# Performance work log

Hardware: AMD Instinct MI355X
Metric: run time of the kernel (lower is better)

Reference implementation:

```python
import jax, jax.numpy as jnp
import numpy as np

D_STATE = 16
DT_RANK = 48
D_CONV = 4
EPS = 1e-5


def rmsnorm(x, w):
    return x * jax.lax.rsqrt(jnp.mean(x * x, axis=-1, keepdims=True) + EPS) * w


def causal_dw_conv(u, w, b):
    # u: [B,T,D], w: [D,K] depthwise causal kernel, b: [D]
    B, T, D = u.shape
    K = w.shape[1]
    up = jnp.pad(u, ((0, 0), (K - 1, 0), (0, 0)))
    acc = jnp.zeros_like(u)
    for k in range(K):  # K=4, tiny fixed loop
        acc = acc + up[:, k:k + T, :] * w[:, k]
    return acc + b


def mamba_mixer(h, ipw, cw, cb, xpw, dpw, dpb, alog, dpar, opw):
    # h: [B,T,d_model]
    B, T, _ = h.shape
    xz = h @ ipw.T                       # [B,T,2*d_inner]
    u, z = jnp.split(xz, 2, axis=-1)     # each [B,T,d_inner]
    u = jax.nn.silu(causal_dw_conv(u, cw, cb))
    xp = u @ xpw.T                       # [B,T,dt_rank+2*d_state]
    dt = xp[..., :DT_RANK]
    Bm = xp[..., DT_RANK:DT_RANK + D_STATE]
    Cm = xp[..., DT_RANK + D_STATE:]
    delta = jax.nn.softplus(dt @ dpw.T + dpb)      # [B,T,d_inner]
    A = -jnp.exp(alog)                              # [d_inner, d_state], negative
    dA = jnp.exp(delta[..., None] * A)              # [B,T,d_inner,d_state] in (0,1)
    dBu = (delta * u)[..., None] * Bm[:, :, None, :]
    # time-major for scan
    dA_t = jnp.moveaxis(dA, 1, 0)
    dBu_t = jnp.moveaxis(dBu, 1, 0)
    C_t = jnp.moveaxis(Cm, 1, 0)

    def step(hst, inp):
        a, bu, c = inp
        hst = a * hst + bu                          # [B,d_inner,d_state]
        y = jnp.einsum('bdn,bn->bd', hst, c)
        return hst, y

    h0 = jnp.zeros((B, u.shape[-1], D_STATE), u.dtype)
    _, ys = jax.lax.scan(step, h0, (dA_t, dBu_t, C_t))
    y = jnp.moveaxis(ys, 0, 1) + u * dpar           # skip via D
    y = y * jax.nn.silu(z)                          # gate
    return y @ opw.T                                # [B,T,d_model]


def setup_inputs() -> dict:
    key = jax.random.key(0)
    ks = jax.random.split(key, 16)
    L, d_model, d_inner = 4, 768, 1536
    B, C, T = 4, 256, 512
    s = 0.02
    return {
        'x': jax.random.normal(ks[0], (B, C, T), jnp.float32),
        'in_proj_w': jax.random.normal(ks[1], (L, 2 * d_inner, d_model), jnp.float32) * s,
        'conv_w': jax.random.normal(ks[2], (L, d_inner, D_CONV), jnp.float32) * 0.3,
        'conv_b': jnp.zeros((L, d_inner), jnp.float32),
        'x_proj_w': jax.random.normal(ks[3], (L, DT_RANK + 2 * D_STATE, d_inner), jnp.float32) * s,
        'dt_proj_w': jax.random.normal(ks[4], (L, d_inner, DT_RANK), jnp.float32) * 0.1,
        'dt_proj_b': jax.random.normal(ks[5], (L, d_inner), jnp.float32) * 0.1 - 4.0,
        'A_log': jax.random.uniform(ks[6], (L, d_inner, D_STATE), jnp.float32, 0.0, 1.5),
        'D_param': jax.random.uniform(ks[7], (L, d_inner), jnp.float32),
        'out_proj_w': jax.random.normal(ks[8], (L, d_model, d_inner), jnp.float32) * s,
        'norm_w': jnp.ones((L, d_model), jnp.float32),
        'norm_f_w': jnp.ones((d_model,), jnp.float32),
        'inp_w': jax.random.normal(ks[9], (d_model, C), jnp.float32) * s,
        'inp_b': jnp.zeros((d_model,), jnp.float32),
        'cls_w': jax.random.normal(ks[10], (10, d_model), jnp.float32) * s,
        'cls_b': jnp.zeros((10,), jnp.float32),
    }


def reference(x, in_proj_w, conv_w, conv_b, x_proj_w, dt_proj_w, dt_proj_b,
              A_log, D_param, out_proj_w, norm_w, norm_f_w,
              inp_w, inp_b, cls_w, cls_b):
    # x: (B, C, T) -> (B, T, C)
    xt = jnp.transpose(x, (0, 2, 1))
    h = xt @ inp_w.T + inp_b                # [B,T,d_model]
    hidden = h
    residual = None
    L = in_proj_w.shape[0]
    for l in range(L):
        residual = hidden if residual is None else hidden + residual
        normed = rmsnorm(residual, norm_w[l])
        hidden = mamba_mixer(normed, in_proj_w[l], conv_w[l], conv_b[l],
                             x_proj_w[l], dt_proj_w[l], dt_proj_b[l],
                             A_log[l], D_param[l], out_proj_w[l])
    residual = hidden + residual
    hidden = rmsnorm(residual, norm_f_w)
    pooled = hidden.mean(axis=1)            # [B,d_model]
    logits = pooled @ cls_w.T + cls_b       # [B,num_labels]
    return logits
```

## Files before the change

kernel.cpp:

```cpp
#include <hip/hip_runtime.h>
#include <math.h>

#define D_MODEL 768
#define D_INNER 1536
#define B_SZ 4
#define T_SZ 512
#define ROWS (B_SZ*T_SZ)
#define XP_N 80
#define CH 16
#define CT 32
#define XS 8
#define XKC (D_INNER/XS)
#define OS 4
#define OKC (D_INNER/OS)
#define MN_OUT (ROWS*768)

typedef __attribute__((ext_vector_type(8))) short bf16x8;
typedef __attribute__((ext_vector_type(4))) float f32x4;

#define GLL(g, l) __builtin_amdgcn_global_load_lds( \
    (const __attribute__((address_space(1))) void*)(g), \
    (__attribute__((address_space(3))) void*)(l), 16, 0, 0)

__device__ __forceinline__ float sigmoidf_(float x){ return 1.0f/(1.0f+__expf(-x)); }
__device__ __forceinline__ float siluf_(float x){ return x*sigmoidf_(x); }
__device__ __forceinline__ unsigned short f2bf(float f){
  unsigned u = __builtin_bit_cast(unsigned, f);
  u = (u + 0x7FFFu + ((u >> 16) & 1u)) >> 16;
  return (unsigned short)u;
}
__device__ __forceinline__ ushort4 cvt4(float4 v){
  ushort4 r; r.x=f2bf(v.x); r.y=f2bf(v.y); r.z=f2bf(v.z); r.w=f2bf(v.w); return r;
}

#define CA_N0 9437184LL
#define CA_N1 4718592LL
#define CA_N2 196608LL
#define CA_N3 786432LL
#define CA_N4 393216LL
__global__ __launch_bounds__(256) void cast_all(
    const float* __restrict__ ipw, unsigned short* __restrict__ wbi,
    const float* __restrict__ opw, unsigned short* __restrict__ wbo,
    const float* __restrict__ inpw, unsigned short* __restrict__ inpwb,
    const float* __restrict__ xpw, unsigned short* __restrict__ xpwb,
    const float* __restrict__ dtw, unsigned short* __restrict__ dtwb)
{
  long long i4 = ((long long)blockIdx.x*256 + threadIdx.x)*4;
  if (i4 < CA_N0){ *(ushort4*)(wbi + i4) = cvt4(*(const float4*)(ipw + i4)); return; }
  i4 -= CA_N0;
  if (i4 < CA_N1){ *(ushort4*)(wbo + i4) = cvt4(*(const float4*)(opw + i4)); return; }
  i4 -= CA_N1;
  if (i4 < CA_N2){ *(ushort4*)(inpwb + i4) = cvt4(*(const float4*)(inpw + i4)); return; }
  i4 -= CA_N2;
  if (i4 < CA_N3){
    const long long l = i4 / (128*1536), rem = i4 % (128*1536);
    const long long r = rem / 1536, k = rem % 1536;
    ushort4 o;
    if (r < 80) o = cvt4(*(const float4*)(xpw + (l*80 + r)*1536 + k));
    else { o.x=0;o.y=0;o.z=0;o.w=0; }
    *(ushort4*)(xpwb + i4) = o; return;
  }
  i4 -= CA_N3;
  if (i4 < CA_N4){
    const long long l = i4 / (1536*64), rem = i4 % (1536*64);
    const long long r = rem / 64, c = rem % 64;
    ushort4 o;
    if (c < 48) o = cvt4(*(const float4*)(dtw + (l*1536 + r)*48 + c));
    else { o.x=0;o.y=0;o.z=0;o.w=0; }
    *(ushort4*)(dtwb + i4) = o;
  }
}

__global__ void transpose_x(const float* __restrict__ x, unsigned short* __restrict__ xtb){
  __shared__ float s[32][33];
  int b = blockIdx.z;
  int t0 = blockIdx.x*32, c0 = blockIdx.y*32;
  int tx = threadIdx.x, ty = threadIdx.y;
  s[ty][tx] = x[((size_t)b*256 + (c0+ty))*512 + (t0+tx)];
  __syncthreads();
  xtb[((size_t)b*512 + (t0+ty))*256 + (c0+tx)] = f2bf(s[tx][ty]);
}

__global__ __launch_bounds__(256) void gemm_bf16(
    const unsigned short* __restrict__ A, const unsigned short* __restrict__ Wb,
    const float* __restrict__ bias,
    float* __restrict__ C, int M, int N, int K)
{
  __shared__ unsigned short As[128*32];
  __shared__ unsigned short Ws[128*32];
  const int tid = threadIdx.x;
  const int bm = blockIdx.y*128, bn = blockIdx.x*128;
  const int wave = tid >> 6, lane = tid & 63;
  const int wm = (wave >> 1)*64, wn = (wave & 1)*64;
  const int fr = lane & 15, quad = lane >> 4;
  f32x4 acc[4][4] = {};
  const int row0 = (wave*64 + lane) >> 2;
  const int khp  = lane & 3;
  const int khl  = (khp + 4 - ((row0 >> 1) & 3)) & 3;
  const unsigned short* Ag = A  + (size_t)(bm + row0)*K + khl*8;
  const unsigned short* Wg = Wb + (size_t)(bn + row0)*K + khl*8;
  const size_t rstep = (size_t)64*K;
  unsigned short* ldsA = As + wave*512;
  unsigned short* ldsW = Ws + wave*512;

  for (int k0 = 0; k0 < K; k0 += 32){
    GLL(Ag + k0,          ldsA);
    GLL(Ag + rstep + k0,  ldsA + 2048);
    GLL(Wg + k0,          ldsW);
    GLL(Wg + rstep + k0,  ldsW + 2048);
    __syncthreads();
    bf16x8 a[4], b[4];
    #pragma unroll
    for (int i=0;i<4;i++){
      const int row = wm + i*16 + fr;
      a[i] = *(const bf16x8*)(As + row*32 + (((quad + (row>>1)) & 3)*8));
    }
    #pragma unroll
    for (int j=0;j<4;j++){
      const int row = wn + j*16 + fr;
      b[j] = *(const bf16x8*)(Ws + row*32 + (((quad + (row>>1)) & 3)*8));
    }
    #pragma unroll
    for (int i=0;i<4;i++)
      #pragma unroll
      for (int j=0;j<4;j++)
        acc[i][j] = __builtin_amdgcn_mfma_f32_16x16x32_bf16(a[i], b[j], acc[i][j], 0, 0, 0);
    __syncthreads();
  }
  #pragma unroll
  for (int i=0;i<4;i++){
    #pragma unroll
    for (int r=0;r<4;r++){
      const int row = bm + wm + i*16 + quad*4 + r;
      float* Cp = C + (size_t)row*N + bn + wn + fr;
      #pragma unroll
      for (int j=0;j<4;j++){
        const int col = bn + wn + j*16 + fr;
        Cp[j*16] = acc[i][j][r] + (bias ? bias[col] : 0.f);
      }
    }
  }
}

__global__ __launch_bounds__(256) void gemm_bf16_sk(
    const unsigned short* __restrict__ A, const unsigned short* __restrict__ Wb,
    float* __restrict__ P0, float* __restrict__ P1, int M, int N, int K)
{
  __shared__ unsigned short As[128*32];
  __shared__ unsigned short Ws[128*32];
  const int tid = threadIdx.x;
  const int bm = blockIdx.y*128, bn = blockIdx.x*128;
  const int s = blockIdx.z;
  const int koff = s*OKC;
  const int wave = tid >> 6, lane = tid & 63;
  const int wm = (wave >> 1)*64, wn = (wave & 1)*64;
  const int fr = lane & 15, quad = lane >> 4;
  f32x4 acc[4][4] = {};
  const int row0 = (wave*64 + lane) >> 2;
  const int khp  = lane & 3;
  const int khl  = (khp + 4 - ((row0 >> 1) & 3)) & 3;
  const unsigned short* Ag = A  + (size_t)(bm + row0)*K + koff + khl*8;
  const unsigned short* Wg = Wb + (size_t)(bn + row0)*K + koff + khl*8;
  const size_t rstep = (size_t)64*K;
  unsigned short* ldsA = As + wave*512;
  unsigned short* ldsW = Ws + wave*512;

  for (int k0 = 0; k0 < OKC; k0 += 32){
    GLL(Ag + k0,          ldsA);
    GLL(Ag + rstep + k0,  ldsA + 2048);
    GLL(Wg + k0,          ldsW);
    GLL(Wg + rstep + k0,  ldsW + 2048);
    __syncthreads();
    bf16x8 a[4], b[4];
    #pragma unroll
    for (int i=0;i<4;i++){
      const int row = wm + i*16 + fr;
      a[i] = *(const bf16x8*)(As + row*32 + (((quad + (row>>1)) & 3)*8));
    }
    #pragma unroll
    for (int j=0;j<4;j++){
      const int row = wn + j*16 + fr;
      b[j] = *(const bf16x8*)(Ws + row*32 + (((quad + (row>>1)) & 3)*8));
    }
    #pragma unroll
    for (int i=0;i<4;i++)
      #pragma unroll
      for (int j=0;j<4;j++)
        acc[i][j] = __builtin_amdgcn_mfma_f32_16x16x32_bf16(a[i], b[j], acc[i][j], 0, 0, 0);
    __syncthreads();
  }
  float* Cb = (s < 2 ? P0 : P1) + (size_t)(s & 1)*MN_OUT;
  #pragma unroll
  for (int i=0;i<4;i++){
    #pragma unroll
    for (int r=0;r<4;r++){
      const int row = bm + wm + i*16 + quad*4 + r;
      float* Cp = Cb + (size_t)row*N + bn + wn + fr;
      #pragma unroll
      for (int j=0;j<4;j++)
        Cp[j*16] = acc[i][j][r];
    }
  }
}

__global__ __launch_bounds__(256) void gemm_bf16_xp(
    const unsigned short* __restrict__ A, const unsigned short* __restrict__ Wb,
    float* __restrict__ part)
{
  __shared__ unsigned short As[128*32];
  __shared__ unsigned short Ws[128*32];
  const int tid = threadIdx.x;
  const int bm = blockIdx.x*128;
  const int s = blockIdx.y;
  const int koff = s*XKC;
  const int wave = tid >> 6, lane = tid & 63;
  const int wm = (wave >> 1)*64, wn = (wave & 1)*64;
  const int fr = lane & 15, quad = lane >> 4;
  f32x4 acc[4][4] = {};
  const int row0 = (wave*64 + lane) >> 2;
  const int khp  = lane & 3;
  const int khl  = (khp + 4 - ((row0 >> 1) & 3)) & 3;
  const unsigned short* Ag = A  + (size_t)(bm + row0)*D_INNER + koff + khl*8;
  const unsigned short* Wg = Wb + (size_t)row0*D_INNER + koff + khl*8;
  const size_t rstep = (size_t)64*D_INNER;
  unsigned short* ldsA = As + wave*512;
  unsigned short* ldsW = Ws + wave*512;

  for (int k0 = 0; k0 < XKC; k0 += 32){
    GLL(Ag + k0,          ldsA);
    GLL(Ag + rstep + k0,  ldsA + 2048);
    GLL(Wg + k0,          ldsW);
    GLL(Wg + rstep + k0,  ldsW + 2048);
    __syncthreads();
    bf16x8 a[4], b[4];
    #pragma unroll
    for (int i=0;i<4;i++){
      const int row = wm + i*16 + fr;
      a[i] = *(const bf16x8*)(As + row*32 + (((quad + (row>>1)) & 3)*8));
    }
    #pragma unroll
    for (int j=0;j<4;j++){
      const int row = wn + j*16 + fr;
      b[j] = *(const bf16x8*)(Ws + row*32 + (((quad + (row>>1)) & 3)*8));
    }
    #pragma unroll
    for (int i=0;i<4;i++)
      #pragma unroll
      for (int j=0;j<4;j++)
        acc[i][j] = __builtin_amdgcn_mfma_f32_16x16x32_bf16(a[i], b[j], acc[i][j], 0, 0, 0);
    __syncthreads();
  }
  #pragma unroll
  for (int i=0;i<4;i++){
    #pragma unroll
    for (int r=0;r<4;r++){
      const int row = bm + wm + i*16 + quad*4 + r;
      #pragma unroll
      for (int j=0;j<4;j++){
        const int col = wn + j*16 + fr;
        if (col < XP_N)
          part[((size_t)s*ROWS + row)*XP_N + col] = acc[i][j][r];
      }
    }
  }
}

__global__ __launch_bounds__(256) void reduce_xp(const float* __restrict__ part,
                                                 float* __restrict__ xp,
                                                 unsigned short* __restrict__ xpb){
  const int i = blockIdx.x*256 + threadIdx.x;
  if (i >= ROWS*XP_N) return;
  const int row = i / XP_N, c = i % XP_N;
  float s = 0.f;
  #pragma unroll
  for (int k=0;k<XS;k++) s += part[(size_t)k*ROWS*XP_N + i];
  xp[i] = s;
  if (c < 48) xpb[row*64 + c] = f2bf(s);
  else if (c < 64) xpb[row*64 + c] = 0;
}

__global__ __launch_bounds__(256) void gemm_bf16_dt(
    const unsigned short* __restrict__ A, const unsigned short* __restrict__ Wb,
    const float* __restrict__ bias, float* __restrict__ C)
{
  __shared__ unsigned short As[128*32];
  __shared__ unsigned short Ws[128*32];
  const int tid = threadIdx.x;
  const int bm = blockIdx.y*128, bn = blockIdx.x*128;
  const int wave = tid >> 6, lane = tid & 63;
  const int wm = (wave >> 1)*64, wn = (wave & 1)*64;
  const int fr = lane & 15, quad = lane >> 4;
  f32x4 acc[4][4] = {};
  const int row0 = (wave*64 + lane) >> 2;
  const int khp  = lane & 3;
  const int khl  = (khp + 4 - ((row0 >> 1) & 3)) & 3;
  const unsigned short* Ag = A  + (size_t)(bm + row0)*64 + khl*8;
  const unsigned short* Wg = Wb + (size_t)(bn + row0)*64 + khl*8;
  const size_t rstepA = (size_t)64*64;
  unsigned short* ldsA = As + wave*512;
  unsigned short* ldsW = Ws + wave*512;

  for (int k0 = 0; k0 < 64; k0 += 32){
    GLL(Ag + k0,           ldsA);
    GLL(Ag + rstepA + k0,  ldsA + 2048);
    GLL(Wg + k0,           ldsW);
    GLL(Wg + rstepA + k0,  ldsW + 2048);
    __syncthreads();
    bf16x8 a[4], b[4];
    #pragma unroll
    for (int i=0;i<4;i++){
      const int row = wm + i*16 + fr;
      a[i] = *(const bf16x8*)(As + row*32 + (((quad + (row>>1)) & 3)*8));
    }
    #pragma unroll
    for (int j=0;j<4;j++){
      const int row = wn + j*16 + fr;
      b[j] = *(const bf16x8*)(Ws + row*32 + (((quad + (row>>1)) & 3)*8));
    }
    #pragma unroll
    for (int i=0;i<4;i++)
      #pragma unroll
      for (int j=0;j<4;j++)
        acc[i][j] = __builtin_amdgcn_mfma_f32_16x16x32_bf16(a[i], b[j], acc[i][j], 0, 0, 0);
    __syncthreads();
  }
  #pragma unroll
  for (int i=0;i<4;i++){
    #pragma unroll
    for (int r=0;r<4;r++){
      const int row = bm + wm + i*16 + quad*4 + r;
      float* Cp = C + (size_t)row*D_INNER + bn + wn + fr;
      #pragma unroll
      for (int j=0;j<4;j++){
        const int col = bn + wn + j*16 + fr;
        float v = acc[i][j][r] + bias[col];
        v = (v > 20.f) ? v : log1pf(__expf(v));
        Cp[j*16] = v;
      }
    }
  }
}

__global__ __launch_bounds__(256) void fused_norm(
    float* __restrict__ resid, const float* __restrict__ P0, const float* __restrict__ P1,
    const float* __restrict__ w, unsigned short* __restrict__ obf, float* __restrict__ ofp)
{
  const int row = blockIdx.x;
  const int tid = threadIdx.x;
  float v[3];
  float ss = 0.f;
  #pragma unroll
  for (int i=0;i<3;i++){
    const int c = tid + i*256;
    const size_t idx = (size_t)row*768 + c;
    float r = resid[idx];
    if (P0) r += (P0[idx] + P0[MN_OUT + idx]) + (P1[idx] + P1[MN_OUT + idx]);
    v[i] = r;
    ss += r*r;
  }
  #pragma unroll
  for (int off=32; off>=1; off>>=1) ss += __shfl_xor(ss, off);
  __shared__ float sred[4];
  const int lane = tid & 63, wv = tid >> 6;
  if (lane == 0) sred[wv] = ss;
  __syncthreads();
  const float tot = sred[0]+sred[1]+sred[2]+sred[3];
  const float scale = rsqrtf(tot*(1.0f/768.0f) + 1e-5f);
  #pragma unroll
  for (int i=0;i<3;i++){
    const int c = tid + i*256;
    const size_t idx = (size_t)row*768 + c;
    if (P0) resid[idx] = v[i];
    const float o = v[i]*scale*w[c];
    if (obf) obf[idx] = f2bf(o);
    else     ofp[idx] = o;
  }
}

__global__ __launch_bounds__(256) void conv_silu(
    const float* __restrict__ xz, const float* __restrict__ cw,
    const float* __restrict__ cb, float* __restrict__ uo,
    unsigned short* __restrict__ ub)
{
  const int idx = blockIdx.x*256 + threadIdx.x;
  if (idx >= ROWS*D_INNER) return;
  const int d = idx % D_INNER;
  const int row = idx / D_INNER;
  const int t = row & (T_SZ-1);
  float acc = cb[d];
  #pragma unroll
  for (int k=0;k<4;k++){
    const int tt = t - 3 + k;
    if (tt >= 0)
      acc += xz[(size_t)(row - 3 + k)*3072 + d] * cw[d*4 + k];
  }
  const float s = siluf_(acc);
  uo[idx] = s;
  ub[idx] = f2bf(s);
}

__global__ __launch_bounds__(256) void scan_pass1(
    const float* __restrict__ delta, const float* __restrict__ u,
    const float* __restrict__ xp, const float* __restrict__ alog,
    float* __restrict__ Pend, float* __restrict__ Hend)
{
  const int d = blockIdx.x*256 + threadIdx.x;
  const int b = blockIdx.y, c = blockIdx.z;
  float4 t0 = *(const float4*)(alog + d*16 + 0);
  float4 t1 = *(const float4*)(alog + d*16 + 4);
  float4 t2 = *(const float4*)(alog + d*16 + 8);
  float4 t3 = *(const float4*)(alog + d*16 + 12);
  float Av[16] = {t0.x,t0.y,t0.z,t0.w,t1.x,t1.y,t1.z,t1.w,
                  t2.x,t2.y,t2.z,t2.w,t3.x,t3.y,t3.z,t3.w};
  float h[16], P[16];
  #pragma unroll
  for (int n=0;n<16;n++){ Av[n] = -__expf(Av[n]); h[n]=0.f; P[n]=1.f; }
  const size_t row0 = (size_t)b*T_SZ + (size_t)c*CT;
  const float* dp = delta + row0*D_INNER + d;
  const float* up = u     + row0*D_INNER + d;
  const float* bp = xp    + row0*XP_N + 48;
  for (int t=0;t<CT;t++){
    const float dv = dp[(size_t)t*D_INNER];
    const float uv = up[(size_t)t*D_INNER];
    const float4 B0 = *(const float4*)(bp + (size_t)t*XP_N);
    const float4 B1 = *(const float4*)(bp + (size_t)t*XP_N + 4);
    const float4 B2 = *(const float4*)(bp + (size_t)t*XP_N + 8);
    const float4 B3 = *(const float4*)(bp + (size_t)t*XP_N + 12);
    const float Bv[16] = {B0.x,B0.y,B0.z,B0.w,B1.x,B1.y,B1.z,B1.w,
                          B2.x,B2.y,B2.z,B2.w,B3.x,B3.y,B3.z,B3.w};
    const float du = dv*uv;
    #pragma unroll
    for (int n=0;n<16;n++){
      const float dA = __expf(dv*Av[n]);
      P[n] *= dA;
      h[n] = dA*h[n] + du*Bv[n];
    }
  }
  float* Pp = Pend + ((size_t)(b*CH+c)*D_INNER + d)*16;
  float* Hp = Hend + ((size_t)(b*CH+c)*D_INNER + d)*16;
  *(float4*)(Pp+ 0) = make_float4(P[0],P[1],P[2],P[3]);
  *(float4*)(Pp+ 4) = make_float4(P[4],P[5],P[6],P[7]);
  *(float4*)(Pp+ 8) = make_float4(P[8],P[9],P[10],P[11]);
  *(float4*)(Pp+12) = make_float4(P[12],P[13],P[14],P[15]);
  *(float4*)(Hp+ 0) = make_float4(h[0],h[1],h[2],h[3]);
  *(float4*)(Hp+ 4) = make_float4(h[4],h[5],h[6],h[7]);
  *(float4*)(Hp+ 8) = make_float4(h[8],h[9],h[10],h[11]);
  *(float4*)(Hp+12) = make_float4(h[12],h[13],h[14],h[15]);
}

__global__ __launch_bounds__(256) void scan_pass3(
    const float* __restrict__ delta, const float* __restrict__ u,
    const float* __restrict__ xp, const float* __restrict__ xz,
    const float* __restrict__ alog, const float* __restrict__ Dp,
    const float* __restrict__ Pend, const float* __restrict__ Hend,
    unsigned short* __restrict__ yb)
{
  const int d = blockIdx.x*256 + threadIdx.x;
  const int b = blockIdx.y, c = blockIdx.z;
  float4 t0 = *(const float4*)(alog + d*16 + 0);
  float4 t1 = *(const float4*)(alog + d*16 + 4);
  float4 t2 = *(const float4*)(alog + d*16 + 8);
  float4 t3 = *(const float4*)(alog + d*16 + 12);
  float Av[16] = {t0.x,t0.y,t0.z,t0.w,t1.x,t1.y,t1.z,t1.w,
                  t2.x,t2.y,t2.z,t2.w,t3.x,t3.y,t3.z,t3.w};
  float h[16];
  #pragma unroll
  for (int n=0;n<16;n++){ Av[n] = -__expf(Av[n]); h[n] = 0.f; }
  for (int cc=0; cc<c; cc++){
    const float* Pp = Pend + ((size_t)(b*CH+cc)*D_INNER + d)*16;
    const float* Hp = Hend + ((size_t)(b*CH+cc)*D_INNER + d)*16;
    float4 p0 = *(const float4*)(Pp+0),  p1 = *(const float4*)(Pp+4);
    float4 p2 = *(const float4*)(Pp+8),  p3 = *(const float4*)(Pp+12);
    float4 q0 = *(const float4*)(Hp+0),  q1 = *(const float4*)(Hp+4);
    float4 q2 = *(const float4*)(Hp+8),  q3 = *(const float4*)(Hp+12);
    const float Pv[16] = {p0.x,p0.y,p0.z,p0.w,p1.x,p1.y,p1.z,p1.w,
                          p2.x,p2.y,p2.z,p2.w,p3.x,p3.y,p3.z,p3.w};
    const float Hv[16] = {q0.x,q0.y,q0.z,q0.w,q1.x,q1.y,q1.z,q1.w,
                          q2.x,q2.y,q2.z,q2.w,q3.x,q3.y,q3.z,q3.w};
    #pragma unroll
    for (int n=0;n<16;n++) h[n] = Pv[n]*h[n] + Hv[n];
  }
  const float Dv = Dp[d];
  const size_t row0 = (size_t)b*T_SZ + (size_t)c*CT;
  const float* dp = delta + row0*D_INNER + d;
  const float* up = u     + row0*D_INNER + d;
  const float* bp = xp    + row0*XP_N + 48;
  const float* cp = xp    + row0*XP_N + 64;
  const float* zp = xz    + row0*3072 + 1536 + d;
  unsigned short* yp = yb + row0*D_INNER + d;
  for (int t=0;t<CT;t++){
    const float dv = dp[(size_t)t*D_INNER];
    const float uv = up[(size_t)t*D_INNER];
    const float zv = zp[(size_t)t*3072];
    const float4 B0 = *(const float4*)(bp + (size_t)t*XP_N);
    const float4 B1 = *(const float4*)(bp + (size_t)t*XP_N + 4);
    const float4 B2 = *(const float4*)(bp + (size_t)t*XP_N + 8);
    const float4 B3 = *(const float4*)(bp + (size_t)t*XP_N + 12);
    const float4 C0 = *(const float4*)(cp + (size_t)t*XP_N);
    const float4 C1 = *(const float4*)(cp + (size_t)t*XP_N + 4);
    const float4 C2 = *(const float4*)(cp + (size_t)t*XP_N + 8);
    const float4 C3 = *(const float4*)(cp + (size_t)t*XP_N + 12);
    const float Bv[16] = {B0.x,B0.y,B0.z,B0.w,B1.x,B1.y,B1.z,B1.w,
                          B2.x,B2.y,B2.z,B2.w,B3.x,B3.y,B3.z,B3.w};
    const float Cv[16] = {C0.x,C0.y,C0.z,C0.w,C1.x,C1.y,C1.z,C1.w,
                          C2.x,C2.y,C2.z,C2.w,C3.x,C3.y,C3.z,C3.w};
    const float du = dv*uv;
    float p = 0.f;
    #pragma unroll
    for (int n=0;n<16;n++){
      const float dA = __expf(dv*Av[n]);
      h[n] = dA*h[n] + du*Bv[n];
      p += h[n]*Cv[n];
    }
    yp[(size_t)t*D_INNER] = f2bf((p + uv*Dv)*siluf_(zv));
  }
}

__global__ __launch_bounds__(256) void pool_partial(const float* __restrict__ normed,
                                                    float* __restrict__ part){
  const int i = blockIdx.x*256 + threadIdx.x;
  const int s = blockIdx.y;
  const int b = i / 768, m = i % 768;
  float sum = 0.f;
  const float* p = normed + ((size_t)b*T_SZ + s*32)*768 + m;
  #pragma unroll
  for (int t=0; t<32; t++) sum += p[(size_t)t*768];
  part[s*3072 + i] = sum;
}

__global__ __launch_bounds__(256) void pool_cls(const float* __restrict__ part,
                                                const float* __restrict__ cw,
                                                const float* __restrict__ cb,
                                                float* __restrict__ out){
  __shared__ float ls[768];
  const int b = blockIdx.x;
  const int tid = threadIdx.x;
  #pragma unroll
  for (int i=0;i<3;i++){
    const int m = tid + i*256;
    float s = 0.f;
    #pragma unroll
    for (int c=0;c<16;c++) s += part[c*3072 + b*768 + m];
    ls[m] = s * (1.0f/T_SZ);
  }
  __syncthreads();
  const int wave = tid >> 6, lane = tid & 63;
  for (int o = wave; o < 10; o += 4){
    float s = 0.f;
    for (int k = lane; k < 768; k += 64) s += ls[k]*cw[o*768 + k];
    #pragma unroll
    for (int off=32; off>=1; off>>=1) s += __shfl_xor(s, off);
    if (lane == 0) out[b*10 + o] = s + cb[o];
  }
}

extern "C" void kernel_launch(void* const* d_in, const int* in_sizes, int n_in,
                              void* d_out, int out_size, void* d_ws, size_t ws_size,
                              hipStream_t stream) {
  const float* x         = (const float*)d_in[0];
  const float* in_proj_w = (const float*)d_in[1];
  const float* conv_w    = (const float*)d_in[2];
  const float* conv_b    = (const float*)d_in[3];
  const float* x_proj_w  = (const float*)d_in[4];
  const float* dt_proj_w = (const float*)d_in[5];
  const float* dt_proj_b = (const float*)d_in[6];
  const float* A_log     = (const float*)d_in[7];
  const float* D_param   = (const float*)d_in[8];
  const float* out_proj_w= (const float*)d_in[9];
  const float* norm_w    = (const float*)d_in[10];
  const float* norm_f_w  = (const float*)d_in[11];
  const float* inp_w     = (const float*)d_in[12];
  const float* inp_b     = (const float*)d_in[13];
  const float* cls_w     = (const float*)d_in[14];
  const float* cls_b     = (const float*)d_in[15];
  float* out = (float*)d_out;

  char* ws = (char*)d_ws;
  auto carve = [&](size_t nelem)->float* {
    float* p = (float*)ws;
    ws += ((nelem*sizeof(float) + 255)/256)*256;
    return p;
  };
  float* xtb_f  = carve((size_t)ROWS*256/2);
  float* resid  = carve((size_t)ROWS*768);
  float* normed = carve((size_t)ROWS*768);
  float* hidden = carve((size_t)ROWS*768);
  float* xz     = carve((size_t)ROWS*3072);
  float* ucv    = carve((size_t)ROWS*1536);
  float* xp     = carve((size_t)ROWS*XP_N);
  float* delta  = carve((size_t)ROWS*1536);
  float* ybf_f  = carve((size_t)ROWS*1536/2);
  float* ubf_f  = carve((size_t)ROWS*1536/2);
  float* xpb_f  = carve((size_t)ROWS*64/2);
  float* wbi_f  = carve((size_t)CA_N0/2);
  float* wbo_f  = carve((size_t)CA_N1/2);
  float* wip_f  = carve((size_t)CA_N2/2);
  float* wxp_f  = carve((size_t)CA_N3/2);
  float* wdt_f  = carve((size_t)CA_N4/2);
  float* xpart  = carve((size_t)XS*ROWS*XP_N);
  float* ppool  = carve((size_t)16*3072);

  unsigned short* xtb = (unsigned short*)xtb_f;
  unsigned short* normedb = (unsigned short*)normed;
  unsigned short* ybf = (unsigned short*)ybf_f;
  unsigned short* ubf = (unsigned short*)ubf_f;
  unsigned short* xpb = (unsigned short*)xpb_f;
  unsigned short* wbi = (unsigned short*)wbi_f;
  unsigned short* wbo = (unsigned short*)wbo_f;
  unsigned short* wip = (unsigned short*)wip_f;
  unsigned short* wxp = (unsigned short*)wxp_f;
  unsigned short* wdt = (unsigned short*)wdt_f;
  float* Pend = normed;
  float* Hend = hidden;

  cast_all<<<15168, 256, 0, stream>>>(in_proj_w, wbi, out_proj_w, wbo,
                                      inp_w, wip, x_proj_w, wxp, dt_proj_w, wdt);
  transpose_x<<<dim3(16,8,4), dim3(32,32), 0, stream>>>(x, xtb);
  gemm_bf16<<<dim3(6,16), 256, 0, stream>>>(xtb, wip, inp_b, resid, ROWS, 768, 256);

  for (int l = 0; l < 4; l++){
    fused_norm<<<2048, 256, 0, stream>>>(resid, l ? delta : nullptr, l ? ucv : nullptr,
                                         norm_w + (size_t)l*768, normedb, nullptr);
    gemm_bf16<<<dim3(24,16), 256, 0, stream>>>(normedb, wbi + (size_t)l*3072*768, nullptr,
                                               xz, ROWS, 3072, 768);
    conv_silu<<<(ROWS*D_INNER)/256, 256, 0, stream>>>(xz, conv_w + (size_t)l*1536*4,
                                                      conv_b + (size_t)l*1536, ucv, ubf);
    gemm_bf16_xp<<<dim3(16,XS), 256, 0, stream>>>(ubf, wxp + (size_t)l*128*1536, xpart);
    reduce_xp<<<(ROWS*XP_N)/256, 256, 0, stream>>>(xpart, xp, xpb);
    gemm_bf16_dt<<<dim3(12,16), 256, 0, stream>>>(xpb, wdt + (size_t)l*1536*64,
                                                  dt_proj_b + (size_t)l*1536, delta);
    scan_pass1<<<dim3(6,B_SZ,CH-1), 256, 0, stream>>>(delta, ucv, xp,
                                               A_log + (size_t)l*1536*16, Pend, Hend);
    scan_pass3<<<dim3(6,B_SZ,CH), 256, 0, stream>>>(delta, ucv, xp, xz,
                                               A_log + (size_t)l*1536*16, D_param + (size_t)l*1536,
                                               Pend, Hend, ybf);
    gemm_bf16_sk<<<dim3(6,16,OS), 256, 0, stream>>>(ybf, wbo + (size_t)l*768*1536,
                                                    delta, ucv, ROWS, 768, 1536);
  }

  fused_norm<<<2048, 256, 0, stream>>>(resid, delta, ucv, norm_f_w, nullptr, normed);
  pool_partial<<<dim3(12,16), 256, 0, stream>>>(normed, ppool);
  pool_cls<<<4, 256, 0, stream>>>(ppool, cls_w, cls_b, out);
}
```

Baseline: 830.8 us.

## Fuse conv+SiLU into x_proj GEMM, reduce into dt GEMM, store xz as bf16

The in_proj GEMM now writes xz in bf16, which halves that buffer's traffic. The depthwise conv and SiLU are recomputed inside the x_proj GEMM prologue, where they fill LDS directly, and again inside both scan passes. This removes the conv_silu kernel and the fp32 u buffer. The split-K xp reduction and the bf16 cast move into the dt GEMM prologue, with softplus applied in its epilogue, which removes reduce_xp; the cost is redundant reduction across N-blocks and some conv recomputation.

```diff
diff --git a/kernel.cpp b/kernel.cpp
--- a/kernel.cpp
+++ b/kernel.cpp
@@ -28,6 +28,9 @@
   unsigned u = __builtin_bit_cast(unsigned, f);
   u = (u + 0x7FFFu + ((u >> 16) & 1u)) >> 16;
   return (unsigned short)u;
+}
+__device__ __forceinline__ float bf2f(unsigned short v){
+  return __builtin_bit_cast(float, (unsigned)v << 16);
 }
 __device__ __forceinline__ ushort4 cvt4(float4 v){
   ushort4 r; r.x=f2bf(v.x); r.y=f2bf(v.y); r.z=f2bf(v.z); r.w=f2bf(v.w); return r;
@@ -81,10 +84,9 @@
   xtb[((size_t)b*512 + (t0+ty))*256 + (c0+tx)] = f2bf(s[tx][ty]);
 }
 
-__global__ __launch_bounds__(256) void gemm_bf16(
+__global__ __launch_bounds__(256) void gemm_input(
     const unsigned short* __restrict__ A, const unsigned short* __restrict__ Wb,
-    const float* __restrict__ bias,
-    float* __restrict__ C, int M, int N, int K)
+    const float* __restrict__ bias, float* __restrict__ C)
 {
   __shared__ unsigned short As[128*32];
   __shared__ unsigned short Ws[128*32];
@@ -95,15 +97,13 @@
   const int fr = lane & 15, quad = lane >> 4;
   f32x4 acc[4][4] = {};
   const int row0 = (wave*64 + lane) >> 2;
-  const int khp  = lane & 3;
-  const int khl  = (khp + 4 - ((row0 >> 1) & 3)) & 3;
-  const unsigned short* Ag = A  + (size_t)(bm + row0)*K + khl*8;
-  const unsigned short* Wg = Wb + (size_t)(bn + row0)*K + khl*8;
-  const size_t rstep = (size_t)64*K;
+  const int khl  = ((lane & 3) + 4 - ((row0 >> 1) & 3)) & 3;
+  const unsigned short* Ag = A  + (size_t)(bm + row0)*256 + khl*8;
+  const unsigned short* Wg = Wb + (size_t)(bn + row0)*256 + khl*8;
+  const size_t rstep = (size_t)64*256;
   unsigned short* ldsA = As + wave*512;
   unsigned short* ldsW = Ws + wave*512;
-
-  for (int k0 = 0; k0 < K; k0 += 32){
+  for (int k0 = 0; k0 < 256; k0 += 32){
     GLL(Ag + k0,          ldsA);
     GLL(Ag + rstep + k0,  ldsA + 2048);
     GLL(Wg + k0,          ldsW);
@@ -128,23 +128,251 @@
     __syncthreads();
   }
   #pragma unroll
-  for (int i=0;i<4;i++){
+  for (int i=0;i<4;i++)
     #pragma unroll
     for (int r=0;r<4;r++){
       const int row = bm + wm + i*16 + quad*4 + r;
-      float* Cp = C + (size_t)row*N + bn + wn + fr;
       #pragma unroll
       for (int j=0;j<4;j++){
         const int col = bn + wn + j*16 + fr;
-        Cp[j*16] = acc[i][j][r] + (bias ? bias[col] : 0.f);
+        C[(size_t)row*768 + col] = acc[i][j][r] + bias[col];
       }
     }
-  }
+}
+
+__global__ __launch_bounds__(256) void gemm_inproj(
+    const unsigned short* __restrict__ A, const unsigned short* __restrict__ Wb,
+    unsigned short* __restrict__ Cb)
+{
+  __shared__ unsigned short As[128*32];
+  __shared__ unsigned short Ws[128*32];
+  const int tid = threadIdx.x;
+  const int bm = blockIdx.y*128, bn = blockIdx.x*128;
+  const int wave = tid >> 6, lane = tid & 63;
+  const int wm = (wave >> 1)*64, wn = (wave & 1)*64;
+  const int fr = lane & 15, quad = lane >> 4;
+  f32x4 acc[4][4] = {};
+  const int row0 = (wave*64 + lane) >> 2;
+  const int khl  = ((lane & 3) + 4 - ((row0 >> 1) & 3)) & 3;
+  const unsigned short* Ag = A  + (size_t)(bm + row0)*768 + khl*8;
+  const unsigned short* Wg = Wb + (size_t)(bn + row0)*768 + khl*8;
+  const size_t rstep = (size_t)64*768;
+  unsigned short* ldsA = As + wave*512;
+  unsigned short* ldsW = Ws + wave*512;
+  for (int k0 = 0; k0 < 768; k0 += 32){
+    GLL(Ag + k0,          ldsA);
+    GLL(Ag + rstep + k0,  ldsA + 2048);
+    GLL(Wg + k0,          ldsW);
+    GLL(Wg + rstep + k0,  ldsW + 2048);
+    __syncthreads();
+    bf16x8 a[4], b[4];
+    #pragma unroll
+    for (int i=0;i<4;i++){
+      const int row = wm + i*16 + fr;
+      a[i] = *(const bf16x8*)(As + row*32 + (((quad + (row>>1)) & 3)*8));
+    }
+    #pragma unroll
+    for (int j=0;j<4;j++){
+      const int row = wn + j*16 + fr;
+      b[j] = *(const bf16x8*)(Ws + row*32 + (((quad + (row>>1)) & 3)*8));
+    }
+    #pragma unroll
+    for (int i=0;i<4;i++)
+      #pragma unroll
+      for (int j=0;j<4;j++)
+        acc[i][j] = __builtin_amdgcn_mfma_f32_16x16x32_bf16(a[i], b[j], acc[i][j], 0, 0, 0);
+    __syncthreads();
+  }
+  #pragma unroll
+  for (int i=0;i<4;i++)
+    #pragma unroll
+    for (int r=0;r<4;r++){
+      const int row = bm + wm + i*16 + quad*4 + r;
+      #pragma unroll
+      for (int j=0;j<4;j++){
+        const int col = bn + wn + j*16 + fr;
+        Cb[(size_t)row*3072 + col] = f2bf(acc[i][j][r]);
+      }
+    }
+}
+
+__global__ __launch_bounds__(256) void gemm_xp_fused(
+    const unsigned short* __restrict__ xzb, const float* __restrict__ cw,
+    const float* __restrict__ cb, const unsigned short* __restrict__ Wl,
+    float* __restrict__ part)
+{
+  __shared__ unsigned short AsAll[6*128*32];
+  __shared__ unsigned short Ws[128*32];
+  const int tid = threadIdx.x;
+  const int bm = blockIdx.x*128;
+  const int s  = blockIdx.y;
+  const int koff = s*XKC;
+  for (int task = tid; task < 128*24; task += 256){
+    const int rl = task / 24, c8 = task % 24;
+    const int r = bm + rl;
+    const int t = r & (T_SZ-1);
+    const int d0 = koff + c8*8;
+    float acc[8];
+    float4 cb0 = *(const float4*)(cb + d0);
+    float4 cb1 = *(const float4*)(cb + d0 + 4);
+    acc[0]=cb0.x; acc[1]=cb0.y; acc[2]=cb0.z; acc[3]=cb0.w;
+    acc[4]=cb1.x; acc[5]=cb1.y; acc[6]=cb1.z; acc[7]=cb1.w;
+    float4 cwv[8];
+    #pragma unroll
+    for (int j=0;j<8;j++) cwv[j] = *(const float4*)(cw + (size_t)(d0+j)*4);
+    #pragma unroll
+    for (int k=0;k<4;k++){
+      const int tt = t - 3 + k;
+      if (tt >= 0){
+        bf16x8 xv = *(const bf16x8*)(xzb + (size_t)(r-3+k)*3072 + d0);
+        #pragma unroll
+        for (int j=0;j<8;j++)
+          acc[j] += bf2f((unsigned short)xv[j]) * ((const float*)&cwv[j])[k];
+      }
+    }
+    bf16x8 ov;
+    #pragma unroll
+    for (int j=0;j<8;j++) ov[j] = (short)f2bf(siluf_(acc[j]));
+    const int kk = c8 >> 2, khl = c8 & 3;
+    const int khp = (khl + (rl >> 1)) & 3;
+    *(bf16x8*)(AsAll + kk*4096 + rl*32 + khp*8) = ov;
+  }
+  const int wave = tid >> 6, lane = tid & 63;
+  const int wm = (wave >> 1)*64, wn = (wave & 1)*64;
+  const int fr = lane & 15, quad = lane >> 4;
+  const int row0 = (wave*64 + lane) >> 2;
+  const int khl2 = ((lane & 3) + 4 - ((row0 >> 1) & 3)) & 3;
+  const unsigned short* Wg = Wl + (size_t)row0*D_INNER + koff + khl2*8;
+  const size_t rstepW = (size_t)64*D_INNER;
+  unsigned short* ldsW = Ws + wave*512;
+  f32x4 accm[4][4] = {};
+  for (int k0 = 0; k0 < XKC; k0 += 32){
+    GLL(Wg + k0,           ldsW);
+    GLL(Wg + rstepW + k0,  ldsW + 2048);
+    __syncthreads();
+    const unsigned short* Ak = AsAll + (k0 >> 5)*4096;
+    bf16x8 a[4], b[4];
+    #pragma unroll
+    for (int i=0;i<4;i++){
+      const int row = wm + i*16 + fr;
+      a[i] = *(const bf16x8*)(Ak + row*32 + (((quad + (row>>1)) & 3)*8));
+    }
+    #pragma unroll
+    for (int j=0;j<4;j++){
+      const int row = wn + j*16 + fr;
+      b[j] = *(const bf16x8*)(Ws + row*32 + (((quad + (row>>1)) & 3)*8));
+    }
+    #pragma unroll
+    for (int i=0;i<4;i++)
+      #pragma unroll
+      for (int j=0;j<4;j++)
+        accm[i][j] = __builtin_amdgcn_mfma_f32_16x16x32_bf16(a[i], b[j], accm[i][j], 0, 0, 0);
+    __syncthreads();
+  }
+  #pragma unroll
+  for (int i=0;i<4;i++)
+    #pragma unroll
+    for (int r=0;r<4;r++){
+      const int row = bm + wm + i*16 + quad*4 + r;
+      #pragma unroll
+      for (int j=0;j<4;j++){
+        const int col = wn + j*16 + fr;
+        if (col < XP_N)
+          part[((size_t)s*ROWS + row)*XP_N + col] = accm[i][j][r];
+      }
+    }
+}
+
+__global__ __launch_bounds__(256) void gemm_dt_fused(
+    const float* __restrict__ xpart, const unsigned short* __restrict__ Wl,
+    const float* __restrict__ bias, float* __restrict__ xp, float* __restrict__ delta)
+{
+  __shared__ unsigned short AsAll[2*128*32];
+  __shared__ unsigned short Ws[128*32];
+  const int tid = threadIdx.x;
+  const int bn = blockIdx.x*128, bm = blockIdx.y*128;
+  {
+    bf16x8 zv = {0,0,0,0,0,0,0,0};
+    for (int i = tid; i < 1024; i += 256) *(bf16x8*)(AsAll + i*8) = zv;
+  }
+  __syncthreads();
+  for (int task = tid; task < 128*10; task += 256){
+    const int rl = task / 10, c8 = task % 10;
+    const int row = bm + rl;
+    const int col0 = c8*8;
+    float4 sa = make_float4(0.f,0.f,0.f,0.f), sb = make_float4(0.f,0.f,0.f,0.f);
+    #pragma unroll
+    for (int k=0;k<XS;k++){
+      const float* pp = xpart + ((size_t)k*ROWS + row)*XP_N + col0;
+      float4 a = *(const float4*)pp;
+      float4 b = *(const float4*)(pp + 4);
+      sa.x+=a.x; sa.y+=a.y; sa.z+=a.z; sa.w+=a.w;
+      sb.x+=b.x; sb.y+=b.y; sb.z+=b.z; sb.w+=b.w;
+    }
+    if (c8 < 6){
+      bf16x8 ov;
+      ov[0]=(short)f2bf(sa.x); ov[1]=(short)f2bf(sa.y); ov[2]=(short)f2bf(sa.z); ov[3]=(short)f2bf(sa.w);
+      ov[4]=(short)f2bf(sb.x); ov[5]=(short)f2bf(sb.y); ov[6]=(short)f2bf(sb.z); ov[7]=(short)f2bf(sb.w);
+      const int kk = c8 >> 2, khl = c8 & 3;
+      const int khp = (khl + (rl >> 1)) & 3;
+      *(bf16x8*)(AsAll + kk*4096 + rl*32 + khp*8) = ov;
+    }
+    if (bn == 0){
+      *(float4*)(xp + (size_t)row*XP_N + col0)     = sa;
+      *(float4*)(xp + (size_t)row*XP_N + col0 + 4) = sb;
+    }
+  }
+  const int wave = tid >> 6, lane = tid & 63;
+  const int wm = (wave >> 1)*64, wn = (wave & 1)*64;
+  const int fr = lane & 15, quad = lane >> 4;
+  const int row0 = (wave*64 + lane) >> 2;
+  const int khl2 = ((lane & 3) + 4 - ((row0 >> 1) & 3)) & 3;
+  const unsigned short* Wg = Wl + (size_t)(bn + row0)*64 + khl2*8;
+  const size_t rstepW = (size_t)64*64;
+  unsigned short* ldsW = Ws + wave*512;
+  f32x4 accm[4][4] = {};
+  for (int k0 = 0; k0 < 64; k0 += 32){
+    GLL(Wg + k0,           ldsW);
+    GLL(Wg + rstepW + k0,  ldsW + 2048);
+    __syncthreads();
+    const unsigned short* Ak = AsAll + (k0 >> 5)*4096;
+    bf16x8 a[4], b[4];
+    #pragma unroll
+    for (int i=0;i<4;i++){
+      const int row = wm + i*16 + fr;
+      a[i] = *(const bf16x8*)(Ak + row*32 + (((quad + (row>>1)) & 3)*8));
+    }
+    #pragma unroll
+    for (int j=0;j<4;j++){
+      const int row = wn + j*16 + fr;
+      b[j] = *(const bf16x8*)(Ws + row*32 + (((quad + (row>>1)) & 3)*8));
+    }
+    #pragma unroll
+    for (int i=0;i<4;i++)
+      #pragma unroll
+      for (int j=0;j<4;j++)
+        accm[i][j] = __builtin_amdgcn_mfma_f32_16x16x32_bf16(a[i], b[j], accm[i][j], 0, 0, 0);
+    __syncthreads();
+  }
+  #pragma unroll
+  for (int i=0;i<4;i++)
+    #pragma unroll
+    for (int r=0;r<4;r++){
+      const int row = bm + wm + i*16 + quad*4 + r;
+      float* Cp = delta + (size_t)row*D_INNER + bn + wn + fr;
+      #pragma unroll
+      for (int j=0;j<4;j++){
+        const int col = bn + wn + j*16 + fr;
+        float v = accm[i][j][r] + bias[col];
+        v = (v > 20.f) ? v : log1pf(__expf(v));
+        Cp[j*16] = v;
+      }
+    }
 }
 
 __global__ __launch_bounds__(256) void gemm_bf16_sk(
     const unsigned short* __restrict__ A, const unsigned short* __restrict__ Wb,
-    float* __restrict__ P0, float* __restrict__ P1, int M, int N, int K)
+    float* __restrict__ P0, float* __restrict__ P1)
 {
   __shared__ unsigned short As[128*32];
   __shared__ unsigned short Ws[128*32];
@@ -157,14 +385,12 @@
   const int fr = lane & 15, quad = lane >> 4;
   f32x4 acc[4][4] = {};
   const int row0 = (wave*64 + lane) >> 2;
-  const int khp  = lane & 3;
-  const int khl  = (khp + 4 - ((row0 >> 1) & 3)) & 3;
-  const unsigned short* Ag = A  + (size_t)(bm + row0)*K + koff + khl*8;
-  const unsigned short* Wg = Wb + (size_t)(bn + row0)*K + koff + khl*8;
-  const size_t rstep = (size_t)64*K;
+  const int khl  = ((lane & 3) + 4 - ((row0 >> 1) & 3)) & 3;
+  const unsigned short* Ag = A  + (size_t)(bm + row0)*1536 + koff + khl*8;
+  const unsigned short* Wg = Wb + (size_t)(bn + row0)*1536 + koff + khl*8;
+  const size_t rstep = (size_t)64*1536;
   unsigned short* ldsA = As + wave*512;
   unsigned short* ldsW = Ws + wave*512;
-
   for (int k0 = 0; k0 < OKC; k0 += 32){
     GLL(Ag + k0,          ldsA);
     GLL(Ag + rstep + k0,  ldsA + 2048);
@@ -189,156 +415,17 @@
         acc[i][j] = __builtin_amdgcn_mfma_f32_16x16x32_bf16(a[i], b[j], acc[i][j], 0, 0, 0);
     __syncthreads();
   }
-  float* Cb = (s < 2 ? P0 : P1) + (size_t)(s & 1)*MN_OUT;
-  #pragma unroll
-  for (int i=0;i<4;i++){
+  float* Cbuf = (s < 2 ? P0 : P1) + (size_t)(s & 1)*MN_OUT;
+  #pragma unroll
+  for (int i=0;i<4;i++)
     #pragma unroll
     for (int r=0;r<4;r++){
       const int row = bm + wm + i*16 + quad*4 + r;
-      float* Cp = Cb + (size_t)row*N + bn + wn + fr;
+      float* Cp = Cbuf + (size_t)row*768 + bn + wn + fr;
       #pragma unroll
       for (int j=0;j<4;j++)
         Cp[j*16] = acc[i][j][r];
     }
-  }
-}
-
-__global__ __launch_bounds__(256) void gemm_bf16_xp(
-    const unsigned short* __restrict__ A, const unsigned short* __restrict__ Wb,
-    float* __restrict__ part)
-{
-  __shared__ unsigned short As[128*32];
-  __shared__ unsigned short Ws[128*32];
-  const int tid = threadIdx.x;
-  const int bm = blockIdx.x*128;
-  const int s = blockIdx.y;
-  const int koff = s*XKC;
-  const int wave = tid >> 6, lane = tid & 63;
-  const int wm = (wave >> 1)*64, wn = (wave & 1)*64;
-  const int fr = lane & 15, quad = lane >> 4;
-  f32x4 acc[4][4] = {};
-  const int row0 = (wave*64 + lane) >> 2;
-  const int khp  = lane & 3;
-  const int khl  = (khp + 4 - ((row0 >> 1) & 3)) & 3;
-  const unsigned short* Ag = A  + (size_t)(bm + row0)*D_INNER + koff + khl*8;
-  const unsigned short* Wg = Wb + (size_t)row0*D_INNER + koff + khl*8;
-  const size_t rstep = (size_t)64*D_INNER;
-  unsigned short* ldsA = As + wave*512;
-  unsigned short* ldsW = Ws + wave*512;
-
-  for (int k0 = 0; k0 < XKC; k0 += 32){
-    GLL(Ag + k0,          ldsA);
-    GLL(Ag + rstep + k0,  ldsA + 2048);
-    GLL(Wg + k0,          ldsW);
-    GLL(Wg + rstep + k0,  ldsW + 2048);
-    __syncthreads();
-    bf16x8 a[4], b[4];
-    #pragma unroll
-    for (int i=0;i<4;i++){
-      const int row = wm + i*16 + fr;
-      a[i] = *(const bf16x8*)(As + row*32 + (((quad + (row>>1)) & 3)*8));
-    }
-    #pragma unroll
-    for (int j=0;j<4;j++){
-      const int row = wn + j*16 + fr;
-      b[j] = *(const bf16x8*)(Ws + row*32 + (((quad + (row>>1)) & 3)*8));
-    }
-    #pragma unroll
-    for (int i=0;i<4;i++)
-      #pragma unroll
-      for (int j=0;j<4;j++)
-        acc[i][j] = __builtin_amdgcn_mfma_f32_16x16x32_bf16(a[i], b[j], acc[i][j], 0, 0, 0);
-    __syncthreads();
-  }
-  #pragma unroll
-  for (int i=0;i<4;i++){
-    #pragma unroll
-    for (int r=0;r<4;r++){
-      const int row = bm + wm + i*16 + quad*4 + r;
-      #pragma unroll
-      for (int j=0;j<4;j++){
-        const int col = wn + j*16 + fr;
-        if (col < XP_N)
-          part[((size_t)s*ROWS + row)*XP_N + col] = acc[i][j][r];
-      }
-    }
-  }
-}
-
-__global__ __launch_bounds__(256) void reduce_xp(const float* __restrict__ part,
-                                                 float* __restrict__ xp,
-                                                 unsigned short* __restrict__ xpb){
-  const int i = blockIdx.x*256 + threadIdx.x;
-  if (i >= ROWS*XP_N) return;
-  const int row = i / XP_N, c = i % XP_N;
-  float s = 0.f;
-  #pragma unroll
-  for (int k=0;k<XS;k++) s += part[(size_t)k*ROWS*XP_N + i];
-  xp[i] = s;
-  if (c < 48) xpb[row*64 + c] = f2bf(s);
-  else if (c < 64) xpb[row*64 + c] = 0;
-}
-
-__global__ __launch_bounds__(256) void gemm_bf16_dt(
-    const unsigned short* __restrict__ A, const unsigned short* __restrict__ Wb,
-    const float* __restrict__ bias, float* __restrict__ C)
-{
-  __shared__ unsigned short As[128*32];
-  __shared__ unsigned short Ws[128*32];
-  const int tid = threadIdx.x;
-  const int bm = blockIdx.y*128, bn = blockIdx.x*128;
-  const int wave = tid >> 6, lane = tid & 63;
-  const int wm = (wave >> 1)*64, wn = (wave & 1)*64;
-  const int fr = lane & 15, quad = lane >> 4;
-  f32x4 acc[4][4] = {};
-  const int row0 = (wave*64 + lane) >> 2;
-  const int khp  = lane & 3;
-  const int khl  = (khp + 4 - ((row0 >> 1) & 3)) & 3;
-  const unsigned short* Ag = A  + (size_t)(bm + row0)*64 + khl*8;
-  const unsigned short* Wg = Wb + (size_t)(bn + row0)*64 + khl*8;
-  const size_t rstepA = (size_t)64*64;
-  unsigned short* ldsA = As + wave*512;
-  unsigned short* ldsW = Ws + wave*512;
-
-  for (int k0 = 0; k0 < 64; k0 += 32){
-    GLL(Ag + k0,           ldsA);
-    GLL(Ag + rstepA + k0,  ldsA + 2048);
-    GLL(Wg + k0,           ldsW);
-    GLL(Wg + rstepA + k0,  ldsW + 2048);
-    __syncthreads();
-    bf16x8 a[4], b[4];
-    #pragma unroll
-    for (int i=0;i<4;i++){
-      const int row = wm + i*16 + fr;
-      a[i] = *(const bf16x8*)(As + row*32 + (((quad + (row>>1)) & 3)*8));
-    }
-    #pragma unroll
-    for (int j=0;j<4;j++){
-      const int row = wn + j*16 + fr;
-      b[j] = *(const bf16x8*)(Ws + row*32 + (((quad + (row>>1)) & 3)*8));
-    }
-    #pragma unroll
-    for (int i=0;i<4;i++)
-      #pragma unroll
-      for (int j=0;j<4;j++)
-        acc[i][j] = __builtin_amdgcn_mfma_f32_16x16x32_bf16(a[i], b[j], acc[i][j], 0, 0, 0);
-    __syncthreads();
-  }
-  #pragma unroll
-  for (int i=0;i<4;i++){
-    #pragma unroll
-    for (int r=0;r<4;r++){
-      const int row = bm + wm + i*16 + quad*4 + r;
-      float* Cp = C + (size_t)row*D_INNER + bn + wn + fr;
-      #pragma unroll
-      for (int j=0;j<4;j++){
-        const int col = bn + wn + j*16 + fr;
-        float v = acc[i][j][r] + bias[col];
-        v = (v > 20.f) ? v : log1pf(__expf(v));
-        Cp[j*16] = v;
-      }
-    }
-  }
 }
 
 __global__ __launch_bounds__(256) void fused_norm(
@@ -377,51 +464,39 @@
   }
 }
 
-__global__ __launch_bounds__(256) void conv_silu(
-    const float* __restrict__ xz, const float* __restrict__ cw,
-    const float* __restrict__ cb, float* __restrict__ uo,
-    unsigned short* __restrict__ ub)
-{
-  const int idx = blockIdx.x*256 + threadIdx.x;
-  if (idx >= ROWS*D_INNER) return;
-  const int d = idx % D_INNER;
-  const int row = idx / D_INNER;
-  const int t = row & (T_SZ-1);
-  float acc = cb[d];
-  #pragma unroll
-  for (int k=0;k<4;k++){
-    const int tt = t - 3 + k;
-    if (tt >= 0)
-      acc += xz[(size_t)(row - 3 + k)*3072 + d] * cw[d*4 + k];
-  }
-  const float s = siluf_(acc);
-  uo[idx] = s;
-  ub[idx] = f2bf(s);
-}
-
 __global__ __launch_bounds__(256) void scan_pass1(
-    const float* __restrict__ delta, const float* __restrict__ u,
+    const float* __restrict__ delta, const unsigned short* __restrict__ xzb,
+    const float* __restrict__ cw, const float* __restrict__ cb,
     const float* __restrict__ xp, const float* __restrict__ alog,
     float* __restrict__ Pend, float* __restrict__ Hend)
 {
   const int d = blockIdx.x*256 + threadIdx.x;
   const int b = blockIdx.y, c = blockIdx.z;
-  float4 t0 = *(const float4*)(alog + d*16 + 0);
-  float4 t1 = *(const float4*)(alog + d*16 + 4);
-  float4 t2 = *(const float4*)(alog + d*16 + 8);
-  float4 t3 = *(const float4*)(alog + d*16 + 12);
-  float Av[16] = {t0.x,t0.y,t0.z,t0.w,t1.x,t1.y,t1.z,t1.w,
-                  t2.x,t2.y,t2.z,t2.w,t3.x,t3.y,t3.z,t3.w};
+  float4 t0v = *(const float4*)(alog + d*16 + 0);
+  float4 t1v = *(const float4*)(alog + d*16 + 4);
+  float4 t2v = *(const float4*)(alog + d*16 + 8);
+  float4 t3v = *(const float4*)(alog + d*16 + 12);
+  float Av[16] = {t0v.x,t0v.y,t0v.z,t0v.w,t1v.x,t1v.y,t1v.z,t1v.w,
+                  t2v.x,t2v.y,t2v.z,t2v.w,t3v.x,t3v.y,t3v.z,t3v.w};
   float h[16], P[16];
   #pragma unroll
   for (int n=0;n<16;n++){ Av[n] = -__expf(Av[n]); h[n]=0.f; P[n]=1.f; }
+  const float4 cwv = *(const float4*)(cw + (size_t)d*4);
+  const float cbd = cb[d];
   const size_t row0 = (size_t)b*T_SZ + (size_t)c*CT;
   const float* dp = delta + row0*D_INNER + d;
-  const float* up = u     + row0*D_INNER + d;
   const float* bp = xp    + row0*XP_N + 48;
+  const unsigned short* xzp = xzb + row0*3072 + d;
+  float xm3 = (c > 0) ? bf2f(xzp[-3*3072]) : 0.f;
+  float xm2 = (c > 0) ? bf2f(xzp[-2*3072]) : 0.f;
+  float xm1 = (c > 0) ? bf2f(xzp[-1*3072]) : 0.f;
   for (int t=0;t<CT;t++){
     const float dv = dp[(size_t)t*D_INNER];
-    const float uv = up[(size_t)t*D_INNER];
+    const float xc = bf2f(xzp[(size_t)t*3072]);
+    float ac = cbd;
+    ac += xm3*cwv.x; ac += xm2*cwv.y; ac += xm1*cwv.z; ac += xc*cwv.w;
+    const float uv = siluf_(ac);
+    xm3 = xm2; xm2 = xm1; xm1 = xc;
     const float4 B0 = *(const float4*)(bp + (size_t)t*XP_N);
     const float4 B1 = *(const float4*)(bp + (size_t)t*XP_N + 4);
     const float4 B2 = *(const float4*)(bp + (size_t)t*XP_N + 8);
@@ -449,20 +524,20 @@
 }
 
 __global__ __launch_bounds__(256) void scan_pass3(
-    const float* __restrict__ delta, const float* __restrict__ u,
-    const float* __restrict__ xp, const float* __restrict__ xz,
-    const float* __restrict__ alog, const float* __restrict__ Dp,
-    const float* __restrict__ Pend, const float* __restrict__ Hend,
-    unsigned short* __restrict__ yb)
+    const float* __restrict__ delta, const unsigned short* __restrict__ xzb,
+    const float* __restrict__ cw, const float* __restrict__ cb,
+    const float* __restrict__ xp, const float* __restrict__ alog,
+    const float* __restrict__ Dp, const float* __restrict__ Pend,
+    const float* __restrict__ Hend, unsigned short* __restrict__ yb)
 {
   const int d = blockIdx.x*256 + threadIdx.x;
   const int b = blockIdx.y, c = blockIdx.z;
-  float4 t0 = *(const float4*)(alog + d*16 + 0);
-  float4 t1 = *(const float4*)(alog + d*16 + 4);
-  float4 t2 = *(const float4*)(alog + d*16 + 8);
-  float4 t3 = *(const float4*)(alog + d*16 + 12);
-  float Av[16] = {t0.x,t0.y,t0.z,t0.w,t1.x,t1.y,t1.z,t1.w,
-                  t2.x,t2.y,t2.z,t2.w,t3.x,t3.y,t3.z,t3.w};
+  float4 t0v = *(const float4*)(alog + d*16 + 0);
+  float4 t1v = *(const float4*)(alog + d*16 + 4);
+  float4 t2v = *(const float4*)(alog + d*16 + 8);
+  float4 t3v = *(const float4*)(alog + d*16 + 12);
+  float Av[16] = {t0v.x,t0v.y,t0v.z,t0v.w,t1v.x,t1v.y,t1v.z,t1v.w,
+                  t2v.x,t2v.y,t2v.z,t2v.w,t3v.x,t3v.y,t3v.z,t3v.w};
   float h[16];
   #pragma unroll
   for (int n=0;n<16;n++){ Av[n] = -__expf(Av[n]); h[n] = 0.f; }
@@ -481,17 +556,26 @@
     for (int n=0;n<16;n++) h[n] = Pv[n]*h[n] + Hv[n];
   }
   const float Dv = Dp[d];
+  const float4 cwv = *(const float4*)(cw + (size_t)d*4);
+  const float cbd = cb[d];
   const size_t row0 = (size_t)b*T_SZ + (size_t)c*CT;
   const float* dp = delta + row0*D_INNER + d;
-  const float* up = u     + row0*D_INNER + d;
   const float* bp = xp    + row0*XP_N + 48;
   const float* cp = xp    + row0*XP_N + 64;
-  const float* zp = xz    + row0*3072 + 1536 + d;
+  const unsigned short* xzp = xzb + row0*3072 + d;
+  const unsigned short* zp  = xzb + row0*3072 + 1536 + d;
   unsigned short* yp = yb + row0*D_INNER + d;
+  float xm3 = (c > 0) ? bf2f(xzp[-3*3072]) : 0.f;
+  float xm2 = (c > 0) ? bf2f(xzp[-2*3072]) : 0.f;
+  float xm1 = (c > 0) ? bf2f(xzp[-1*3072]) : 0.f;
   for (int t=0;t<CT;t++){
     const float dv = dp[(size_t)t*D_INNER];
-    const float uv = up[(size_t)t*D_INNER];
-    const float zv = zp[(size_t)t*3072];
+    const float xc = bf2f(xzp[(size_t)t*3072]);
+    float ac = cbd;
+    ac += xm3*cwv.x; ac += xm2*cwv.y; ac += xm1*cwv.z; ac += xc*cwv.w;
+    const float uv = siluf_(ac);
+    xm3 = xm2; xm2 = xm1; xm1 = xc;
+    const float zv = bf2f(zp[(size_t)t*3072]);
     const float4 B0 = *(const float4*)(bp + (size_t)t*XP_N);
     const float4 B1 = *(const float4*)(bp + (size_t)t*XP_N + 4);
     const float4 B2 = *(const float4*)(bp + (size_t)t*XP_N + 8);
@@ -585,13 +669,11 @@
   float* resid  = carve((size_t)ROWS*768);
   float* normed = carve((size_t)ROWS*768);
   float* hidden = carve((size_t)ROWS*768);
-  float* xz     = carve((size_t)ROWS*3072);
-  float* ucv    = carve((size_t)ROWS*1536);
+  float* xzb_f  = carve((size_t)ROWS*3072/2);
+  float* pbuf2  = carve((size_t)ROWS*1536);
   float* xp     = carve((size_t)ROWS*XP_N);
   float* delta  = carve((size_t)ROWS*1536);
   float* ybf_f  = carve((size_t)ROWS*1536/2);
-  float* ubf_f  = carve((size_t)ROWS*1536/2);
-  float* xpb_f  = carve((size_t)ROWS*64/2);
   float* wbi_f  = carve((size_t)CA_N0/2);
   float* wbo_f  = carve((size_t)CA_N1/2);
   float* wip_f  = carve((size_t)CA_N2/2);
@@ -602,9 +684,8 @@
 
   unsigned short* xtb = (unsigned short*)xtb_f;
   unsigned short* normedb = (unsigned short*)normed;
+  unsigned short* xzb = (unsigned short*)xzb_f;
   unsigned short* ybf = (unsigned short*)ybf_f;
-  unsigned short* ubf = (unsigned short*)ubf_f;
-  unsigned short* xpb = (unsigned short*)xpb_f;
   unsigned short* wbi = (unsigned short*)wbi_f;
   unsigned short* wbo = (unsigned short*)wbo_f;
   unsigned short* wip = (unsigned short*)wip_f;
@@ -616,29 +697,31 @@
   cast_all<<<15168, 256, 0, stream>>>(in_proj_w, wbi, out_proj_w, wbo,
                                       inp_w, wip, x_proj_w, wxp, dt_proj_w, wdt);
   transpose_x<<<dim3(16,8,4), dim3(32,32), 0, stream>>>(x, xtb);
-  gemm_bf16<<<dim3(6,16), 256, 0, stream>>>(xtb, wip, inp_b, resid, ROWS, 768, 256);
+  gemm_input<<<dim3(6,16), 256, 0, stream>>>(xtb, wip, inp_b, resid);
 
   for (int l = 0; l < 4; l++){
-    fused_norm<<<2048, 256, 0, stream>>>(resid, l ? delta : nullptr, l ? ucv : nullptr,
+    fused_norm<<<2048, 256, 0, stream>>>(resid, l ? delta : nullptr, l ? pbuf2 : nullptr,
                                          norm_w + (size_t)l*768, normedb, nullptr);
-    gemm_bf16<<<dim3(24,16), 256, 0, stream>>>(normedb, wbi + (size_t)l*3072*768, nullptr,
-                                               xz, ROWS, 3072, 768);
-    conv_silu<<<(ROWS*D_INNER)/256, 256, 0, stream>>>(xz, conv_w + (size_t)l*1536*4,
-                                                      conv_b + (size_t)l*1536, ucv, ubf);
-    gemm_bf16_xp<<<dim3(16,XS), 256, 0, stream>>>(ubf, wxp + (size_t)l*128*1536, xpart);
-    reduce_xp<<<(ROWS*XP_N)/256, 256, 0, stream>>>(xpart, xp, xpb);
-    gemm_bf16_dt<<<dim3(12,16), 256, 0, stream>>>(xpb, wdt + (size_t)l*1536*64,
-                                                  dt_proj_b + (size_t)l*1536, delta);
-    scan_pass1<<<dim3(6,B_SZ,CH-1), 256, 0, stream>>>(delta, ucv, xp,
-                                               A_log + (size_t)l*1536*16, Pend, Hend);
-    scan_pass3<<<dim3(6,B_SZ,CH), 256, 0, stream>>>(delta, ucv, xp, xz,
-                                               A_log + (size_t)l*1536*16, D_param + (size_t)l*1536,
-                                               Pend, Hend, ybf);
+    gemm_inproj<<<dim3(24,16), 256, 0, stream>>>(normedb, wbi + (size_t)l*3072*768, xzb);
+    gemm_xp_fused<<<dim3(16,XS), 256, 0, stream>>>(xzb, conv_w + (size_t)l*1536*4,
+                                                   conv_b + (size_t)l*1536,
+                                                   wxp + (size_t)l*128*1536, xpart);
+    gemm_dt_fused<<<dim3(12,16), 256, 0, stream>>>(xpart, wdt + (size_t)l*1536*64,
+                                                   dt_proj_b + (size_t)l*1536, xp, delta);
+    scan_pass1<<<dim3(6,B_SZ,CH-1), 256, 0, stream>>>(delta, xzb,
+                                                      conv_w + (size_t)l*1536*4,
+                                                      conv_b + (size_t)l*1536, xp,
+                                                      A_log + (size_t)l*1536*16, Pend, Hend);
+    scan_pass3<<<dim3(6,B_SZ,CH), 256, 0, stream>>>(delta, xzb,
+                                                    conv_w + (size_t)l*1536*4,
+                                                    conv_b + (size_t)l*1536, xp,
+                                                    A_log + (size_t)l*1536*16,
+                                                    D_param + (size_t)l*1536, Pend, Hend, ybf);
     gemm_bf16_sk<<<dim3(6,16,OS), 256, 0, stream>>>(ybf, wbo + (size_t)l*768*1536,
-                                                    delta, ucv, ROWS, 768, 1536);
-  }
-
-  fused_norm<<<2048, 256, 0, stream>>>(resid, delta, ucv, norm_f_w, nullptr, normed);
+                                                    delta, pbuf2);
+  }
+
+  fused_norm<<<2048, 256, 0, stream>>>(resid, delta, pbuf2, norm_f_w, nullptr, normed);
   pool_partial<<<dim3(12,16), 256, 0, stream>>>(normed, ppool);
   pool_cls<<<4, 256, 0, stream>>>(ppool, cls_w, cls_b, out);
 }
```

Result: slower. 876.2 us (+5.5%).
